# Optimization experiments

Hardware: AMD Instinct MI355X
Metric: run time of the kernel (lower is better)

Reference implementation:

```python
import jax, jax.numpy as jnp
import numpy as np

EMBED_DIM_LIST = [512, 768, 1024]
NUM_HEADS_LIST = [8, 16]
MAX_D_IN = max(EMBED_DIM_LIST)                                        # 1024
MAX_D_OUT = (max(EMBED_DIM_LIST) // min(NUM_HEADS_LIST)) * 3 * max(NUM_HEADS_LIST)  # 6144
BATCH, SEQ = 8, 1024


def _masks():
    # For combo k = (i, j): weight slice is W[:out_k, :in_k] zero-padded to [MAX_D_OUT, MAX_D_IN].
    out_dims = np.array([e // h * 3 * h for e in EMBED_DIM_LIST for h in NUM_HEADS_LIST])  # [K]
    in_dims = np.array([e for e in EMBED_DIM_LIST for h in NUM_HEADS_LIST])                # [K]
    row = (np.arange(MAX_D_OUT)[None, :] < out_dims[:, None]).astype(np.float32)  # [K, D_out]
    col = (np.arange(MAX_D_IN)[None, :] < in_dims[:, None]).astype(np.float32)    # [K, D_in]
    return jnp.asarray(row), jnp.asarray(col)


def setup_inputs() -> dict:
    key = jax.random.key(0)
    k1, k2, k3, k4 = jax.random.split(key, 4)
    K = len(EMBED_DIM_LIST) * len(NUM_HEADS_LIST)
    x = jax.random.normal(k1, (BATCH, SEQ, MAX_D_IN), dtype=jnp.float32)
    weights = jax.random.uniform(k2, (K,), dtype=jnp.float32)
    W = jax.random.normal(k3, (MAX_D_OUT, MAX_D_IN), dtype=jnp.float32) * 0.02
    b = jax.random.normal(k4, (MAX_D_OUT,), dtype=jnp.float32) * 0.02
    return {"x": x, "weights": weights, "W": W, "b": b}


def reference(x, weights, W, b):
    # weights_mix = sum_k weights[k] * pad(W[:out_k, :in_k])
    #             = W * (sum_k weights[k] * row_mask_k[:, None] * col_mask_k[None, :])
    row, col = _masks()                               # [K, D_out], [K, D_in]
    M = jnp.einsum('k,ko,ki->oi', weights, row, col)  # [D_out, D_in] scalar mixing mask
    W_mix = W * M
    b_mix = b * (weights @ row)                       # [D_out]
    # F.linear: x @ W_mix.T + b_mix
    return jnp.einsum('bsi,oi->bso', x, W_mix) + b_mix
```

## Files before the change

kernel.cpp:

```cpp
#include <hip/hip_runtime.h>

typedef unsigned short u16;
typedef __bf16 bf16x8 __attribute__((ext_vector_type(8)));
typedef float f32x4 __attribute__((ext_vector_type(4)));

#define M_DIM 8192
#define K_DIM 1024
#define N_EFF 3072
#define N_FULL 6144
#define BM 128
#define BN 128
#define BK 32

__device__ __forceinline__ u16 f2bf_rne(float f) {
    unsigned u = __float_as_uint(f);
    u += 0x7fffu + ((u >> 16) & 1u);
    return (u16)(u >> 16);
}

__device__ __forceinline__ void gld_lds16(const u16* g, u16* l) {
    __builtin_amdgcn_global_load_lds(
        (const __attribute__((address_space(1))) unsigned int*)g,
        (__attribute__((address_space(3))) unsigned int*)l, 16, 0, 0);
}

__global__ void cvt_x(const float* __restrict__ in, u16* __restrict__ out, int n8) {
    int i = blockIdx.x * 256 + threadIdx.x;
    if (i >= n8) return;
    const float4* p = reinterpret_cast<const float4*>(in) + 2 * (size_t)i;
    float4 a = p[0], b = p[1];
    union { u16 h[8]; uint4 v; } r;
    float vals[8] = {a.x, a.y, a.z, a.w, b.x, b.y, b.z, b.w};
#pragma unroll
    for (int j = 0; j < 8; j++) r.h[j] = f2bf_rne(vals[j]);
    reinterpret_cast<uint4*>(out)[i] = r.v;
}

__global__ void prep_w(const float* __restrict__ W, const float* __restrict__ wt,
                       u16* __restrict__ Wm, int n8) {
    int i = blockIdx.x * 256 + threadIdx.x;
    if (i >= n8) return;
    float w01 = wt[0] + wt[1], w23 = wt[2] + wt[3], w45 = wt[4] + wt[5];
    int o = i >> 7;
    int ib = (i & 127) * 8;
    float s = w45;
    if (o < 2304 && ib < 768) s += w23;
    if (o < 1536 && ib < 512) s += w01;
    const float4* p = reinterpret_cast<const float4*>(W) + 2 * (size_t)i;
    float4 a = p[0], b = p[1];
    union { u16 h[8]; uint4 v; } r;
    float vals[8] = {a.x, a.y, a.z, a.w, b.x, b.y, b.z, b.w};
#pragma unroll
    for (int j = 0; j < 8; j++) r.h[j] = f2bf_rne(vals[j] * s);
    reinterpret_cast<uint4*>(Wm)[i] = r.v;
}

__global__ void prep_b(const float* __restrict__ b, const float* __restrict__ wt,
                       float* __restrict__ bm) {
    int o = blockIdx.x * 256 + threadIdx.x;
    if (o >= N_EFF) return;
    float w01 = wt[0] + wt[1], w23 = wt[2] + wt[3], w45 = wt[4] + wt[5];
    float s = w45 + (o < 2304 ? w23 : 0.f) + (o < 1536 ? w01 : 0.f);
    bm[o] = b[o] * s;
}

__global__ __launch_bounds__(256, 2) void gemm_bt(
    const u16* __restrict__ A,
    const u16* __restrict__ B,
    const float* __restrict__ bias,
    float* __restrict__ C)
{
    __shared__ u16 As[BM * BK];
    __shared__ u16 Bs[BN * BK];

    const int tid  = threadIdx.x;
    const int bx   = blockIdx.x;
    const int by   = blockIdx.y;
    const int lane = tid & 63;
    const int wv   = tid >> 6;
    const int wm   = (wv >> 1) * 64;
    const int wn   = (wv & 1) * 64;

    f32x4 acc[4][4] = {};

    const u16* Ag = A + (size_t)(by * BM) * K_DIM;
    const u16* Bg = B + (size_t)(bx * BN) * K_DIM;

    const int kq  = (lane >> 4) * 8;
    const int r16 = lane & 15;

    for (int kt = 0; kt < K_DIM; kt += BK) {
        __syncthreads();
#pragma unroll
        for (int s = 0; s < 2; s++) {
            int c = s * 256 + tid;
            int row = c >> 2, kc = (c & 3) * 8;
            gld_lds16(Ag + (size_t)row * K_DIM + kt + kc, &As[c * 8]);
            gld_lds16(Bg + (size_t)row * K_DIM + kt + kc, &Bs[c * 8]);
        }
        __syncthreads();

        bf16x8 af[4], bf[4];
#pragma unroll
        for (int t = 0; t < 4; t++) {
            af[t] = *reinterpret_cast<const bf16x8*>(&As[(wm + t * 16 + r16) * BK + kq]);
            bf[t] = *reinterpret_cast<const bf16x8*>(&Bs[(wn + t * 16 + r16) * BK + kq]);
        }
#pragma unroll
        for (int tm = 0; tm < 4; tm++)
#pragma unroll
            for (int tn = 0; tn < 4; tn++)
                acc[tm][tn] = __builtin_amdgcn_mfma_f32_16x16x32_bf16(
                    af[tm], bf[tn], acc[tm][tn], 0, 0, 0);
    }

    const int m0 = by * BM + wm + (lane >> 4) * 4;
    const int n0 = bx * BN + wn + (lane & 15);
#pragma unroll
    for (int tn = 0; tn < 4; tn++) {
        int n = n0 + tn * 16;
        float bv = bias[n];
#pragma unroll
        for (int tm = 0; tm < 4; tm++) {
            int m = m0 + tm * 16;
#pragma unroll
            for (int r = 0; r < 4; r++)
                C[(size_t)(m + r) * N_FULL + n] = acc[tm][tn][r] + bv;
        }
    }

    const float4 z = make_float4(0.f, 0.f, 0.f, 0.f);
#pragma unroll
    for (int it = 0; it < 16; it++) {
        int lin = it * 256 + tid;
        int row = lin >> 5;
        int c4  = (lin & 31) * 4;
        reinterpret_cast<float4*>(
            &C[(size_t)(by * BM + row) * N_FULL + N_EFF + bx * BN + c4])[0] = z;
    }
}

extern "C" void kernel_launch(void* const* d_in, const int* in_sizes, int n_in,
                              void* d_out, int out_size, void* d_ws, size_t ws_size,
                              hipStream_t stream) {
    const float* x   = (const float*)d_in[0];
    const float* wts = (const float*)d_in[1];
    const float* W   = (const float*)d_in[2];
    const float* b   = (const float*)d_in[3];
    float* out = (float*)d_out;

    u16*   xb = (u16*)d_ws;
    u16*   Wm = (u16*)((char*)d_ws + 16777216);
    float* bm = (float*)((char*)d_ws + 23068672);

    cvt_x <<<4096, 256, 0, stream>>>(x, xb, M_DIM * K_DIM / 8);
    prep_w<<<1536, 256, 0, stream>>>(W, wts, Wm, N_EFF * K_DIM / 8);
    prep_b<<<12,   256, 0, stream>>>(b, wts, bm);
    gemm_bt<<<dim3(N_EFF / BN, M_DIM / BM), 256, 0, stream>>>(xb, Wm, bm, out);
}
```

Baseline: 315.1 us.

## Fuse bias prep into GEMM, load two K-steps per barrier, nontemporal stores

Removes the separate prep_b kernel and computes the mixed bias scale inside the GEMM epilogue. The main loop now loads two BK slices into doubled LDS per sync pair, halving barrier count. Output and zero-fill stores become nontemporal, and launch bounds move to 3 blocks per SIMD. Doubling LDS and the higher occupancy target may pressure registers or LDS and limit achievable occupancy.

```diff
diff --git a/kernel.cpp b/kernel.cpp
--- a/kernel.cpp
+++ b/kernel.cpp
@@ -55,23 +55,15 @@
     reinterpret_cast<uint4*>(Wm)[i] = r.v;
 }
 
-__global__ void prep_b(const float* __restrict__ b, const float* __restrict__ wt,
-                       float* __restrict__ bm) {
-    int o = blockIdx.x * 256 + threadIdx.x;
-    if (o >= N_EFF) return;
-    float w01 = wt[0] + wt[1], w23 = wt[2] + wt[3], w45 = wt[4] + wt[5];
-    float s = w45 + (o < 2304 ? w23 : 0.f) + (o < 1536 ? w01 : 0.f);
-    bm[o] = b[o] * s;
-}
-
-__global__ __launch_bounds__(256, 2) void gemm_bt(
+__global__ __launch_bounds__(256, 3) void gemm_bt(
     const u16* __restrict__ A,
     const u16* __restrict__ B,
     const float* __restrict__ bias,
+    const float* __restrict__ wt,
     float* __restrict__ C)
 {
-    __shared__ u16 As[BM * BK];
-    __shared__ u16 Bs[BN * BK];
+    __shared__ u16 As[2 * BM * BK];
+    __shared__ u16 Bs[2 * BN * BK];
 
     const int tid  = threadIdx.x;
     const int bx   = blockIdx.x;
@@ -89,54 +81,66 @@
     const int kq  = (lane >> 4) * 8;
     const int r16 = lane & 15;
 
-    for (int kt = 0; kt < K_DIM; kt += BK) {
+    for (int kt = 0; kt < K_DIM; kt += 2 * BK) {
         __syncthreads();
 #pragma unroll
-        for (int s = 0; s < 2; s++) {
-            int c = s * 256 + tid;
-            int row = c >> 2, kc = (c & 3) * 8;
-            gld_lds16(Ag + (size_t)row * K_DIM + kt + kc, &As[c * 8]);
-            gld_lds16(Bg + (size_t)row * K_DIM + kt + kc, &Bs[c * 8]);
+        for (int u = 0; u < 4; u++) {
+            int c  = u * 256 + tid;
+            int st = c >> 9;
+            int c2 = c & 511;
+            int row = c2 >> 2, kc = (c2 & 3) * 8;
+            size_t goff = (size_t)row * K_DIM + kt + st * BK + kc;
+            gld_lds16(Ag + goff, &As[c * 8]);
+            gld_lds16(Bg + goff, &Bs[c * 8]);
         }
         __syncthreads();
 
-        bf16x8 af[4], bf[4];
 #pragma unroll
-        for (int t = 0; t < 4; t++) {
-            af[t] = *reinterpret_cast<const bf16x8*>(&As[(wm + t * 16 + r16) * BK + kq]);
-            bf[t] = *reinterpret_cast<const bf16x8*>(&Bs[(wn + t * 16 + r16) * BK + kq]);
+        for (int st = 0; st < 2; st++) {
+            bf16x8 af[4], bf[4];
+#pragma unroll
+            for (int t = 0; t < 4; t++) {
+                af[t] = *reinterpret_cast<const bf16x8*>(
+                    &As[st * 4096 + (wm + t * 16 + r16) * BK + kq]);
+                bf[t] = *reinterpret_cast<const bf16x8*>(
+                    &Bs[st * 4096 + (wn + t * 16 + r16) * BK + kq]);
+            }
+#pragma unroll
+            for (int tm = 0; tm < 4; tm++)
+#pragma unroll
+                for (int tn = 0; tn < 4; tn++)
+                    acc[tm][tn] = __builtin_amdgcn_mfma_f32_16x16x32_bf16(
+                        af[tm], bf[tn], acc[tm][tn], 0, 0, 0);
         }
-#pragma unroll
-        for (int tm = 0; tm < 4; tm++)
-#pragma unroll
-            for (int tn = 0; tn < 4; tn++)
-                acc[tm][tn] = __builtin_amdgcn_mfma_f32_16x16x32_bf16(
-                    af[tm], bf[tn], acc[tm][tn], 0, 0, 0);
     }
+
+    const float w01 = wt[0] + wt[1], w23 = wt[2] + wt[3], w45 = wt[4] + wt[5];
 
     const int m0 = by * BM + wm + (lane >> 4) * 4;
     const int n0 = bx * BN + wn + (lane & 15);
 #pragma unroll
     for (int tn = 0; tn < 4; tn++) {
         int n = n0 + tn * 16;
-        float bv = bias[n];
+        float s = w45 + (n < 2304 ? w23 : 0.f) + (n < 1536 ? w01 : 0.f);
+        float bv = bias[n] * s;
 #pragma unroll
         for (int tm = 0; tm < 4; tm++) {
             int m = m0 + tm * 16;
 #pragma unroll
             for (int r = 0; r < 4; r++)
-                C[(size_t)(m + r) * N_FULL + n] = acc[tm][tn][r] + bv;
+                __builtin_nontemporal_store(acc[tm][tn][r] + bv,
+                    &C[(size_t)(m + r) * N_FULL + n]);
         }
     }
 
-    const float4 z = make_float4(0.f, 0.f, 0.f, 0.f);
+    const f32x4 z = {0.f, 0.f, 0.f, 0.f};
 #pragma unroll
     for (int it = 0; it < 16; it++) {
         int lin = it * 256 + tid;
         int row = lin >> 5;
         int c4  = (lin & 31) * 4;
-        reinterpret_cast<float4*>(
-            &C[(size_t)(by * BM + row) * N_FULL + N_EFF + bx * BN + c4])[0] = z;
+        __builtin_nontemporal_store(z, reinterpret_cast<f32x4*>(
+            &C[(size_t)(by * BM + row) * N_FULL + N_EFF + bx * BN + c4]));
     }
 }
 
@@ -149,12 +153,10 @@
     const float* b   = (const float*)d_in[3];
     float* out = (float*)d_out;
 
-    u16*   xb = (u16*)d_ws;
-    u16*   Wm = (u16*)((char*)d_ws + 16777216);
-    float* bm = (float*)((char*)d_ws + 23068672);
+    u16* xb = (u16*)d_ws;
+    u16* Wm = (u16*)((char*)d_ws + 16777216);
 
     cvt_x <<<4096, 256, 0, stream>>>(x, xb, M_DIM * K_DIM / 8);
     prep_w<<<1536, 256, 0, stream>>>(W, wts, Wm, N_EFF * K_DIM / 8);
-    prep_b<<<12,   256, 0, stream>>>(b, wts, bm);
-    gemm_bt<<<dim3(N_EFF / BN, M_DIM / BM), 256, 0, stream>>>(xb, Wm, bm, out);
+    gemm_bt<<<dim3(N_EFF / BN, M_DIM / BM), 256, 0, stream>>>(xb, Wm, b, wts, out);
 }
```

Result: faster. 284.4 us (-9.7%).
